# Kernel optimization log

Measured on AMD Instinct MI355X. Metric: run time of the kernel, lower is better.

Reference implementation:

```python
import jax, jax.numpy as jnp
import numpy as np


def setup_inputs() -> dict:
    key = jax.random.key(0)
    ks = jax.random.split(key, 8)
    H = 256  # hidden_size
    NH = 8   # num_heads
    HD = H // NH
    B, G = 256, 1024
    s = 1.0 / np.sqrt(H)
    return {
        "query": jax.random.normal(ks[0], (B, 2 * H), dtype=jnp.float32),
        "ref": jax.random.normal(ks[1], (B, G, H), dtype=jnp.float32),
        "Wq": jax.random.normal(ks[2], (H, 2 * H), dtype=jnp.float32) * s,
        "bq": jax.random.normal(ks[3], (H,), dtype=jnp.float32) * s,
        "We": jax.random.normal(ks[4], (H, H), dtype=jnp.float32) * s,
        "be": jax.random.normal(ks[5], (H,), dtype=jnp.float32) * s,
        "Wv": jax.random.normal(ks[6], (HD,), dtype=jnp.float32) * (1.0 / np.sqrt(HD)),
        "bv": jax.random.normal(ks[7], (1,), dtype=jnp.float32) * 0.01,
        "num_heads": 8,
    }


def reference(query, ref, Wq, bq, We, be, Wv, bv, num_heads):
    B, G, H = ref.shape
    hd = H // num_heads
    # q_dense: [B, 2H] -> [B, H] -> [B, nh, hd]
    q = (query @ Wq.T + bq).reshape(B, num_heads, hd)
    # e_dense: [B, G, H] -> [B, G, H] -> [B, G, nh, hd]
    e = (jnp.einsum('bgh,oh->bgo', ref, We) + be).reshape(B, G, num_heads, hd)
    # broadcast-add over graph dim, tanh, per-head linear scorer (hd -> 1)
    v = jnp.tanh(q[:, None, :, :] + e)                 # [B, G, nh, hd]
    s = jnp.einsum('bgnd,d->bgn', v, Wv) + bv[0]       # [B, G, nh]
    # sum over heads, output [B, 1, G] (matches sum(dim=1).transpose(1,2))
    return s.sum(axis=-1)[:, None, :]
```

## Files before the change

kernel.cpp:

```cpp
#include <hip/hip_runtime.h>

typedef __attribute__((ext_vector_type(8))) short short8;
typedef __attribute__((ext_vector_type(8))) unsigned short ushort8;
typedef __attribute__((ext_vector_type(4))) float f32x4;
typedef unsigned short ushort;
typedef unsigned int uint;

__device__ __forceinline__ float fast_exp2(float x) {
#if __has_builtin(__builtin_amdgcn_exp2f)
    return __builtin_amdgcn_exp2f(x);
#else
    return __expf(x * 0.6931471805599453f);
#endif
}
__device__ __forceinline__ float fast_rcp(float x) {
#if __has_builtin(__builtin_amdgcn_rcpf)
    return __builtin_amdgcn_rcpf(x);
#else
    return __frcp_rn(x);
#endif
}

__device__ __forceinline__ ushort f2bf(float f) {
    uint x = __float_as_uint(f);
    x += 0x7fffu + ((x >> 16) & 1u);
    return (ushort)(x >> 16);
}

__device__ __forceinline__ uint pack2bf(float x, float y) {
    uint xi = __float_as_uint(x) + 0x8000u;
    uint yi = __float_as_uint(y) + 0x8000u;
    return __builtin_amdgcn_perm(yi, xi, 0x07060302u);
}

__global__ __launch_bounds__(256) void prep(
    const float* __restrict__ query, const float* __restrict__ Wq,
    const float* __restrict__ bq, const float* __restrict__ be,
    const float* __restrict__ We, const float* __restrict__ Wv,
    const float* __restrict__ bv, float* __restrict__ q_ws,
    ushort* __restrict__ Web, float* __restrict__ aux) {
    __shared__ float qrow[512];
    const int t = threadIdx.x;
    if (blockIdx.x < 64) {
        const int i = (blockIdx.x * 256 + t) * 4;
        float4 v = *(const float4*)(We + i);
        ushort4 u;
        u.x = f2bf(v.x); u.y = f2bf(v.y); u.z = f2bf(v.z); u.w = f2bf(v.w);
        *(ushort4*)(Web + i) = u;
        return;
    }
    if (blockIdx.x == 320) {
        if (t >= 64) return;
        float v = (t < 32) ? Wv[t] : 0.f;
#pragma unroll
        for (int off = 1; off < 32; off <<= 1) v += __shfl_xor(v, off, 64);
        if (t == 0) aux[0] = 8.f * (v + bv[0]);
        return;
    }
    const int b = blockIdx.x - 64;
    qrow[t]       = query[b * 512 + t];
    qrow[t + 256] = query[b * 512 + 256 + t];
    __syncthreads();
    const f32x4* wr = (const f32x4*)(Wq + (size_t)t * 512);
    float s0 = 0.f, s1 = 0.f, s2 = 0.f, s3 = 0.f;
#pragma unroll 4
    for (int j = 0; j < 128; j += 4) {
        f32x4 w0 = wr[j], w1 = wr[j + 1], w2 = wr[j + 2], w3 = wr[j + 3];
        f32x4 q0 = *(const f32x4*)(qrow + 4 * j);
        f32x4 q1 = *(const f32x4*)(qrow + 4 * j + 4);
        f32x4 q2 = *(const f32x4*)(qrow + 4 * j + 8);
        f32x4 q3 = *(const f32x4*)(qrow + 4 * j + 12);
        s0 += w0.x * q0.x + w0.y * q0.y + w0.z * q0.z + w0.w * q0.w;
        s1 += w1.x * q1.x + w1.y * q1.y + w1.z * q1.z + w1.w * q1.w;
        s2 += w2.x * q2.x + w2.y * q2.y + w2.z * q2.z + w2.w * q2.w;
        s3 += w3.x * q3.x + w3.y * q3.y + w3.z * q3.z + w3.w * q3.w;
    }
    q_ws[b * 256 + t] = (s0 + s1) + (s2 + s3) + bq[t] + be[t];
}

#define BM 64

__global__ __launch_bounds__(256, 4) void fused_gemm(
    const float* __restrict__ ref, const ushort* __restrict__ Web,
    const float* __restrict__ q_ws, const float* __restrict__ Wv,
    const float* __restrict__ aux, float* __restrict__ out) {
    __shared__ uint4 Asm[2048];
    __shared__ float red[4][64];

    const int t = threadIdx.x;
    const int w = t >> 6;
    const int l = t & 63;
    const int quad = l >> 4;
    const int lr = l & 15;
    const size_t row0 = (size_t)blockIdx.x * BM;
    const int b = (int)(row0 >> 10);

    {
        const float* ap = ref + (row0 + w * 16 + lr) * 256 + quad * 8;
#pragma unroll
        for (int half = 0; half < 2; ++half) {
            float4 f[8];
#pragma unroll
            for (int kb = 0; kb < 4; ++kb) {
                f[2 * kb]     = *(const float4*)(ap + (half * 4 + kb) * 32);
                f[2 * kb + 1] = *(const float4*)(ap + (half * 4 + kb) * 32 + 4);
            }
#pragma unroll
            for (int kb = 0; kb < 4; ++kb) {
                uint4 p;
                p.x = pack2bf(f[2 * kb].x,     f[2 * kb].y);
                p.y = pack2bf(f[2 * kb].z,     f[2 * kb].w);
                p.z = pack2bf(f[2 * kb + 1].x, f[2 * kb + 1].y);
                p.w = pack2bf(f[2 * kb + 1].z, f[2 * kb + 1].w);
                Asm[(w * 8 + half * 4 + kb) * 64 + l] = p;
            }
        }
    }

    const ushort* Bp = Web + ((size_t)(w * 64 + lr)) * 256 + quad * 8;
    short8 bcur[4];
#pragma unroll
    for (int cb = 0; cb < 4; ++cb)
        bcur[cb] = *(const short8*)(Bp + cb * 16 * 256);

    const float c2l = 2.885390081777927f;
    const float* qe = q_ws + b * 256;
    const float w2a = -2.f * Wv[lr];
    const float w2b = -2.f * Wv[16 + lr];
    float qvc[4];
#pragma unroll
    for (int cb = 0; cb < 4; ++cb) qvc[cb] = qe[w * 64 + cb * 16 + lr] * c2l;

    __syncthreads();

    f32x4 acc[4][4];
#pragma unroll
    for (int i = 0; i < 4; ++i)
#pragma unroll
        for (int j = 0; j < 4; ++j) acc[i][j] = (f32x4){0.f, 0.f, 0.f, 0.f};

    const ushort* As = (const ushort*)Asm;
#pragma unroll
    for (int k = 0; k < 8; ++k) {
        short8 bnxt[4];
        if (k < 7) {
#pragma unroll
            for (int cb = 0; cb < 4; ++cb)
                bnxt[cb] = *(const short8*)(Bp + cb * 16 * 256 + (k + 1) * 32);
        }
        short8 afr[4];
#pragma unroll
        for (int rb = 0; rb < 4; ++rb)
            afr[rb] = *(const short8*)(As + ((rb * 8 + k) * 64 + l) * 8);
#pragma unroll
        for (int rb = 0; rb < 4; ++rb)
#pragma unroll
            for (int cb = 0; cb < 4; ++cb)
                acc[rb][cb] = __builtin_amdgcn_mfma_f32_16x16x32_bf16(
                    afr[rb], bcur[cb], acc[rb][cb], 0, 0, 0);
        if (k < 7) {
#pragma unroll
            for (int cb = 0; cb < 4; ++cb) bcur[cb] = bnxt[cb];
        }
    }

    float part[4][4];
#pragma unroll
    for (int rb = 0; rb < 4; ++rb)
#pragma unroll
        for (int r = 0; r < 4; ++r) part[rb][r] = 0.f;

#pragma unroll
    for (int cb = 0; cb < 4; ++cb) {
        const float w2 = (cb & 1) ? w2b : w2a;
#pragma unroll
        for (int rb = 0; rb < 4; ++rb)
#pragma unroll
            for (int r = 0; r < 4; ++r) {
                float e = fast_exp2(fmaf(acc[rb][cb][r], c2l, qvc[cb]));
                part[rb][r] = fmaf(w2, fast_rcp(e + 1.f), part[rb][r]);
            }
    }
#pragma unroll
    for (int off = 1; off < 16; off <<= 1)
#pragma unroll
        for (int rb = 0; rb < 4; ++rb)
#pragma unroll
            for (int r = 0; r < 4; ++r)
                part[rb][r] += __shfl_xor(part[rb][r], off, 64);

    if (lr == 0) {
#pragma unroll
        for (int rb = 0; rb < 4; ++rb)
#pragma unroll
            for (int r = 0; r < 4; ++r)
                red[w][rb * 16 + quad * 4 + r] = part[rb][r];
    }
    __syncthreads();
    if (t < 64) {
        float s = red[0][t] + red[1][t] + red[2][t] + red[3][t] + aux[0];
        out[row0 + t] = s;
    }
}

extern "C" void kernel_launch(void* const* d_in, const int* in_sizes, int n_in,
                              void* d_out, int out_size, void* d_ws, size_t ws_size,
                              hipStream_t stream) {
    const float* query = (const float*)d_in[0];
    const float* ref   = (const float*)d_in[1];
    const float* Wq    = (const float*)d_in[2];
    const float* bq    = (const float*)d_in[3];
    const float* We    = (const float*)d_in[4];
    const float* be    = (const float*)d_in[5];
    const float* Wv    = (const float*)d_in[6];
    const float* bv    = (const float*)d_in[7];
    float* out = (float*)d_out;

    float*  q_ws = (float*)d_ws;
    ushort* Web  = (ushort*)((char*)d_ws + 262144);
    float*  aux  = (float*)((char*)d_ws + 262144 + 131072);

    prep<<<321, 256, 0, stream>>>(query, Wq, bq, be, We, Wv, bv, q_ws, Web, aux);
    fused_gemm<<<4096, 256, 0, stream>>>(ref, Web, q_ws, Wv, aux, out);
}
```

Baseline: 419.4 us.

## Double row tile per block to 128 and pipeline ref loads with bf16 packing

Each block now handles 128 rows instead of 64, so every B-fragment (We in bf16) loaded into registers feeds twice as many MFMAs, and the grid shrinks to 2048 blocks. The ref tile is loaded in four stages with a two-deep register buffer, so global loads overlap the bf16 packing and LDS stores. LDS grows to 64KB and is reused for the reduction buffer, which needs an extra barrier. Launch bounds drop to 2 blocks per CU because accumulator registers double, which reduces occupancy and the latency hiding it gives.

```diff
diff --git a/kernel.cpp b/kernel.cpp
--- a/kernel.cpp
+++ b/kernel.cpp
@@ -1,7 +1,6 @@
 #include <hip/hip_runtime.h>
 
 typedef __attribute__((ext_vector_type(8))) short short8;
-typedef __attribute__((ext_vector_type(8))) unsigned short ushort8;
 typedef __attribute__((ext_vector_type(4))) float f32x4;
 typedef unsigned short ushort;
 typedef unsigned int uint;
@@ -78,43 +77,57 @@
     q_ws[b * 256 + t] = (s0 + s1) + (s2 + s3) + bq[t] + be[t];
 }
 
-#define BM 64
-
-__global__ __launch_bounds__(256, 4) void fused_gemm(
+__global__ __launch_bounds__(256, 2) void fused_gemm(
     const float* __restrict__ ref, const ushort* __restrict__ Web,
     const float* __restrict__ q_ws, const float* __restrict__ Wv,
     const float* __restrict__ aux, float* __restrict__ out) {
-    __shared__ uint4 Asm[2048];
-    __shared__ float red[4][64];
+    __shared__ uint4 Asm[4096];
+    float* red = (float*)Asm;
 
     const int t = threadIdx.x;
     const int w = t >> 6;
     const int l = t & 63;
     const int quad = l >> 4;
     const int lr = l & 15;
-    const size_t row0 = (size_t)blockIdx.x * BM;
+    const size_t row0 = (size_t)blockIdx.x * 128;
     const int b = (int)(row0 >> 10);
 
-    {
-        const float* ap = ref + (row0 + w * 16 + lr) * 256 + quad * 8;
-#pragma unroll
-        for (int half = 0; half < 2; ++half) {
-            float4 f[8];
-#pragma unroll
-            for (int kb = 0; kb < 4; ++kb) {
-                f[2 * kb]     = *(const float4*)(ap + (half * 4 + kb) * 32);
-                f[2 * kb + 1] = *(const float4*)(ap + (half * 4 + kb) * 32 + 4);
+    float4 buf[2][8];
+#pragma unroll
+    for (int pre = 0; pre < 2; ++pre) {
+#pragma unroll
+        for (int j = 0; j < 4; ++j) {
+            const int s = w + 16 * pre + 4 * j;
+            const float* p = ref + (row0 + (s >> 3) * 16 + lr) * 256
+                                 + (s & 7) * 32 + quad * 8;
+            buf[pre][2 * j]     = *(const float4*)p;
+            buf[pre][2 * j + 1] = *(const float4*)(p + 4);
+        }
+    }
+#pragma unroll
+    for (int bt = 0; bt < 4; ++bt) {
+        uint4 pk[4];
+#pragma unroll
+        for (int j = 0; j < 4; ++j) {
+            float4 x = buf[bt & 1][2 * j], y = buf[bt & 1][2 * j + 1];
+            pk[j].x = pack2bf(x.x, x.y);
+            pk[j].y = pack2bf(x.z, x.w);
+            pk[j].z = pack2bf(y.x, y.y);
+            pk[j].w = pack2bf(y.z, y.w);
+        }
+        if (bt < 2) {
+#pragma unroll
+            for (int j = 0; j < 4; ++j) {
+                const int s = w + 16 * (bt + 2) + 4 * j;
+                const float* p = ref + (row0 + (s >> 3) * 16 + lr) * 256
+                                     + (s & 7) * 32 + quad * 8;
+                buf[bt & 1][2 * j]     = *(const float4*)p;
+                buf[bt & 1][2 * j + 1] = *(const float4*)(p + 4);
             }
-#pragma unroll
-            for (int kb = 0; kb < 4; ++kb) {
-                uint4 p;
-                p.x = pack2bf(f[2 * kb].x,     f[2 * kb].y);
-                p.y = pack2bf(f[2 * kb].z,     f[2 * kb].w);
-                p.z = pack2bf(f[2 * kb + 1].x, f[2 * kb + 1].y);
-                p.w = pack2bf(f[2 * kb + 1].z, f[2 * kb + 1].w);
-                Asm[(w * 8 + half * 4 + kb) * 64 + l] = p;
-            }
-        }
+        }
+#pragma unroll
+        for (int j = 0; j < 4; ++j)
+            Asm[(w + 16 * bt + 4 * j) * 64 + l] = pk[j];
     }
 
     const ushort* Bp = Web + ((size_t)(w * 64 + lr)) * 256 + quad * 8;
@@ -133,9 +146,9 @@
 
     __syncthreads();
 
-    f32x4 acc[4][4];
-#pragma unroll
-    for (int i = 0; i < 4; ++i)
+    f32x4 acc[8][4];
+#pragma unroll
+    for (int i = 0; i < 8; ++i)
 #pragma unroll
         for (int j = 0; j < 4; ++j) acc[i][j] = (f32x4){0.f, 0.f, 0.f, 0.f};
 
@@ -148,25 +161,23 @@
             for (int cb = 0; cb < 4; ++cb)
                 bnxt[cb] = *(const short8*)(Bp + cb * 16 * 256 + (k + 1) * 32);
         }
-        short8 afr[4];
-#pragma unroll
-        for (int rb = 0; rb < 4; ++rb)
-            afr[rb] = *(const short8*)(As + ((rb * 8 + k) * 64 + l) * 8);
-#pragma unroll
-        for (int rb = 0; rb < 4; ++rb)
+#pragma unroll
+        for (int rb = 0; rb < 8; ++rb) {
+            short8 afr = *(const short8*)(As + ((rb * 8 + k) * 64 + l) * 8);
 #pragma unroll
             for (int cb = 0; cb < 4; ++cb)
                 acc[rb][cb] = __builtin_amdgcn_mfma_f32_16x16x32_bf16(
-                    afr[rb], bcur[cb], acc[rb][cb], 0, 0, 0);
+                    afr, bcur[cb], acc[rb][cb], 0, 0, 0);
+        }
         if (k < 7) {
 #pragma unroll
             for (int cb = 0; cb < 4; ++cb) bcur[cb] = bnxt[cb];
         }
     }
 
-    float part[4][4];
-#pragma unroll
-    for (int rb = 0; rb < 4; ++rb)
+    float part[8][4];
+#pragma unroll
+    for (int rb = 0; rb < 8; ++rb)
 #pragma unroll
         for (int r = 0; r < 4; ++r) part[rb][r] = 0.f;
 
@@ -174,7 +185,7 @@
     for (int cb = 0; cb < 4; ++cb) {
         const float w2 = (cb & 1) ? w2b : w2a;
 #pragma unroll
-        for (int rb = 0; rb < 4; ++rb)
+        for (int rb = 0; rb < 8; ++rb)
 #pragma unroll
             for (int r = 0; r < 4; ++r) {
                 float e = fast_exp2(fmaf(acc[rb][cb][r], c2l, qvc[cb]));
@@ -184,21 +195,22 @@
 #pragma unroll
     for (int off = 1; off < 16; off <<= 1)
 #pragma unroll
-        for (int rb = 0; rb < 4; ++rb)
+        for (int rb = 0; rb < 8; ++rb)
 #pragma unroll
             for (int r = 0; r < 4; ++r)
                 part[rb][r] += __shfl_xor(part[rb][r], off, 64);
 
+    __syncthreads();
     if (lr == 0) {
 #pragma unroll
-        for (int rb = 0; rb < 4; ++rb)
+        for (int rb = 0; rb < 8; ++rb)
 #pragma unroll
             for (int r = 0; r < 4; ++r)
-                red[w][rb * 16 + quad * 4 + r] = part[rb][r];
-    }
-    __syncthreads();
-    if (t < 64) {
-        float s = red[0][t] + red[1][t] + red[2][t] + red[3][t] + aux[0];
+                red[w * 128 + rb * 16 + quad * 4 + r] = part[rb][r];
+    }
+    __syncthreads();
+    if (t < 128) {
+        float s = red[t] + red[128 + t] + red[256 + t] + red[384 + t] + aux[0];
         out[row0 + t] = s;
     }
 }
@@ -221,5 +233,5 @@
     float*  aux  = (float*)((char*)d_ws + 262144 + 131072);
 
     prep<<<321, 256, 0, stream>>>(query, Wq, bq, be, We, Wv, bv, q_ws, Web, aux);
-    fused_gemm<<<4096, 256, 0, stream>>>(ref, Web, q_ws, Wv, aux, out);
-}
+    fused_gemm<<<2048, 256, 0, stream>>>(ref, Web, q_ws, Wv, aux, out);
+}
```

Result: no change. 425.9 us (+1.5%).
